# Kernel tuning notes

Measured on AMD Instinct MI355X. Metric: run time of the kernel, lower is better.

The kernel has to match this reference:

```python
import jax, jax.numpy as jnp
import numpy as np

B, T, C = 8, 2048, 1024      # batch, timesteps, input_dim
G, E = 2, 320                # groups_dim, entries_dim
EMB = 512                    # emb_dim
D = EMB // G                 # true_emb_dim per group


def setup_inputs() -> dict:
    key = jax.random.key(0)
    k1, k2, k3 = jax.random.split(key, 3)
    X = jax.random.normal(k1, (B, T, C), dtype=jnp.float32)
    # nn.Linear(input_dim, G*E): weight (out,in) ~ N(0,1), bias zeros
    W = jax.random.normal(k2, (G * E, C), dtype=jnp.float32)
    b = jnp.zeros((G * E,), dtype=jnp.float32)
    # codebook Parameter(1, G*E, D) ~ U[0,1); stored squeezed as (G*E, D)
    codebook = jax.random.uniform(k3, (G * E, D), dtype=jnp.float32)
    return {"X": X, "W": W, "b": b, "codebook": codebook}


def reference(X, W, b, codebook):
    # Eval-mode forward of VectorQuantization (time_first=True).
    nB, nT, _ = X.shape
    logits = jnp.einsum("btc,kc->btk", X, W) + b           # (B, T, G*E)
    # Faithful to source: view (B,T,G*E) as (B*G, T*E) and argmax over last dim
    flat = logits.reshape(nB * G, nT * E)                   # (B*G, T*E)
    k = jnp.argmax(flat, axis=-1)                           # (B*G,)
    hard = jax.nn.one_hot(k, nT * E, dtype=logits.dtype)    # (B*G, T*E)
    q = hard.reshape(nB * nT, G, E)                         # (B*T, G, E)
    # (one-hot * codebook).sum over entries == per-group gather
    cb = codebook.reshape(G, E, D)                          # (G, E, D)
    out = jnp.einsum("nge,ged->ngd", q, cb)                 # (B*T, G, D)
    return out.reshape(nB, nT, G * D)                       # (B, T, emb_dim)
```

## Files before the change

### kernel.cpp

```cpp
#include <hip/hip_runtime.h>
#include <stdint.h>

#define CC    1024
#define EE    320
#define KN    640
#define DD    256
#define MTOT  16384
#define NBLK  640
#define OUT4  2097152
#define MARGIN 2.0f

typedef __attribute__((ext_vector_type(8))) short short8;
typedef __attribute__((ext_vector_type(4))) float f32x4;

__device__ __forceinline__ unsigned int f32_orderable(float x) {
    unsigned int b = __float_as_uint(x);
    return (b & 0x80000000u) ? ~b : (b | 0x80000000u);
}

__device__ __forceinline__ unsigned short bf16_rne(float x) {
    unsigned int u = __float_as_uint(x);
    return (unsigned short)((u + 0x7FFFu + ((u >> 16) & 1u)) >> 16);
}

__global__ void init_slots_kernel(unsigned long long* __restrict__ slots) {
    if (threadIdx.x < 17) slots[threadIdx.x] = 0ull;
}

__global__ __launch_bounds__(256)
void convert_kernel(const float* __restrict__ X, const float* __restrict__ W,
                    unsigned short* __restrict__ A2F, unsigned short* __restrict__ B2F,
                    unsigned long long* __restrict__ slots, float* __restrict__ out) {
    const int bid = blockIdx.x;
    const int tid = threadIdx.x;
    {
        int zidx = bid * 256 + tid;
        f32x4 z = {0.f, 0.f, 0.f, 0.f};
        if (zidx < OUT4) __builtin_nontemporal_store(z, (f32x4*)out + zidx);
    }
    const int lane = tid & 63;
    const float* src;
    unsigned short* dst;
    int unit;
    if (bid < 8192) {
        unit = bid * 4 + (tid >> 6);
        src = X; dst = A2F;
    } else {
        if (bid == 8192 && tid < 17) slots[tid] = 0ull;
        unit = (bid - 8192) * 4 + (tid >> 6);
        src = W; dst = B2F;
    }
    int rt = unit >> 5, kc = unit & 31;
    int row = rt * 16 + (lane & 15);
    int col = kc * 32 + ((lane >> 4) << 3);
    const float* p = src + (size_t)row * CC + col;
    float4 v0 = *(const float4*)p;
    float4 v1 = *(const float4*)(p + 4);
    short8 hi;
    hi[0] = (short)bf16_rne(v0.x); hi[1] = (short)bf16_rne(v0.y);
    hi[2] = (short)bf16_rne(v0.z); hi[3] = (short)bf16_rne(v0.w);
    hi[4] = (short)bf16_rne(v1.x); hi[5] = (short)bf16_rne(v1.y);
    hi[6] = (short)bf16_rne(v1.z); hi[7] = (short)bf16_rne(v1.w);
    *(short8*)(dst + (size_t)unit * 512 + lane * 8) = hi;
}

__global__ __launch_bounds__(256, 3)
void gemm_argmax_mfma(const unsigned short* __restrict__ A2F,
                      const unsigned short* __restrict__ B2F,
                      const float* __restrict__ X,
                      const float* __restrict__ W,
                      const float* __restrict__ bias,
                      const float* __restrict__ codebook,
                      float* __restrict__ out,
                      unsigned long long* __restrict__ slots,
                      unsigned int* __restrict__ counter) {
    __shared__ float redf[4];
    __shared__ int cnt_s;
    __shared__ int cand_s[128];
    __shared__ unsigned int done_s;
    __shared__ unsigned long long s16[16];

    const int tid  = threadIdx.x;
    const int lane = tid & 63;
    const int wave = tid >> 6;

    const int l   = blockIdx.x;
    const int xcd = l & 7;
    const int w   = l >> 3;
    const int mt  = xcd * 16 + w / 5;
    const int nt  = w % 5;
    const int m0 = mt * 128;
    const int n0 = nt * 128;

    const int wm = (wave >> 1) * 64;
    const int wn = (wave & 1) * 64;

    const unsigned short* Ap[4];
    const unsigned short* Bp[4];
#pragma unroll
    for (int t = 0; t < 4; t++) {
        Ap[t] = A2F + ((size_t)(((m0 + wm) >> 4) + t) * 32) * 512 + lane * 8;
        Bp[t] = B2F + ((size_t)(((n0 + wn) >> 4) + t) * 32) * 512 + lane * 8;
    }

    f32x4 acc[4][4] = {};
    short8 a0[4], b0[4], a1[4], b1[4];

#pragma unroll
    for (int t = 0; t < 4; t++) {
        a0[t] = *(const short8*)(Ap[t]);
        b0[t] = *(const short8*)(Bp[t]);
        Ap[t] += 512; Bp[t] += 512;
    }

#define STEP(CURA, CURB, NXTA, NXTB, IT)                                         \
    {                                                                            \
        if ((IT) < 31) {                                                         \
            _Pragma("unroll")                                                    \
            for (int t = 0; t < 4; t++) {                                        \
                NXTA[t] = *(const short8*)(Ap[t]);                               \
                NXTB[t] = *(const short8*)(Bp[t]);                               \
                Ap[t] += 512; Bp[t] += 512;                                      \
            }                                                                    \
        }                                                                        \
        _Pragma("unroll")                                                        \
        for (int ti = 0; ti < 4; ti++)                                           \
            _Pragma("unroll")                                                    \
            for (int tj = 0; tj < 4; tj++)                                       \
                acc[ti][tj] = __builtin_amdgcn_mfma_f32_16x16x32_bf16(           \
                    CURA[ti], CURB[tj], acc[ti][tj], 0, 0, 0);                   \
    }

    for (int it2 = 0; it2 < 16; it2++) {
        STEP(a0, b0, a1, b1, it2 * 2)
        STEP(a1, b1, a0, b0, it2 * 2 + 1)
    }
#undef STEP

    float bias4[4];
#pragma unroll
    for (int tj = 0; tj < 4; tj++) bias4[tj] = bias[n0 + wn + tj * 16 + (lane & 15)];

    float vmax = -3.0e38f;
#pragma unroll
    for (int ti = 0; ti < 4; ti++)
#pragma unroll
        for (int tj = 0; tj < 4; tj++)
#pragma unroll
            for (int r = 0; r < 4; r++)
                vmax = fmaxf(vmax, acc[ti][tj][r] + bias4[tj]);
#pragma unroll
    for (int off = 32; off > 0; off >>= 1)
        vmax = fmaxf(vmax, __shfl_down(vmax, off, 64));
    if (lane == 0) redf[wave] = vmax;
    if (tid == 0) cnt_s = 0;
    __syncthreads();
    float bm = fmaxf(fmaxf(redf[0], redf[1]), fmaxf(redf[2], redf[3]));
    float thresh = bm - MARGIN;

#pragma unroll
    for (int ti = 0; ti < 4; ti++) {
#pragma unroll
        for (int r = 0; r < 4; r++) {
            int m = m0 + wm + ti * 16 + (lane >> 4) * 4 + r;
#pragma unroll
            for (int tj = 0; tj < 4; tj++) {
                float v = acc[ti][tj][r] + bias4[tj];
                if (v >= thresh) {
                    int n = n0 + wn + tj * 16 + (lane & 15);
                    int idx = atomicAdd(&cnt_s, 1);
                    if (idx < 128) cand_s[idx] = (m << 10) | n;
                }
            }
        }
    }
    __syncthreads();
    int cnt = cnt_s < 128 ? cnt_s : 128;

    for (int i = 0; i < cnt; i++) {
        int mc = cand_s[i] >> 10;
        int nc = cand_s[i] & 1023;
        float4 xv = *(const float4*)(X + (size_t)mc * CC + tid * 4);
        float4 wv = *(const float4*)(W + (size_t)nc * CC + tid * 4);
        float p = xv.x * wv.x + xv.y * wv.y + xv.z * wv.z + xv.w * wv.w;
#pragma unroll
        for (int off = 32; off > 0; off >>= 1) p += __shfl_down(p, off, 64);
        if (lane == 0) redf[wave] = p;
        __syncthreads();
        if (tid == 0) {
            float tot = redf[0] + redf[1] + redf[2] + redf[3] + bias[nc];
            unsigned int c = (unsigned int)((mc & 1023) * KN + nc);
            unsigned long long pk =
                ((unsigned long long)f32_orderable(tot) << 32) |
                (unsigned long long)(~c);
            atomicMax(slots + (mc >> 10), pk);
        }
        __syncthreads();
    }

    if (tid == 0) {
        __threadfence();
        done_s = atomicAdd(counter, 1u);
    }
    __syncthreads();

    if (done_s == NBLK - 1) {
        if (tid < 16) s16[tid] = atomicAdd(slots + tid, 0ull);
        __syncthreads();
        int rr  = tid >> 4;
        int seg = tid & 15;
        unsigned long long p = s16[rr];
        unsigned int c = ~(unsigned int)(p & 0xFFFFFFFFull);
        int tl = (int)(c / KN);
        int kg = (int)(c % KN);
        int b  = rr >> 1, h = rr & 1;
        int nstar = b * 2048 + h * 1024 + tl;
        int g = kg / EE;
        const float4* src = (const float4*)(codebook + (size_t)kg * DD) + seg * 4;
        float4* dst = (float4*)(out + (size_t)nstar * 512 + (size_t)g * DD) + seg * 4;
#pragma unroll
        for (int j = 0; j < 4; j++) dst[j] = src[j];
    }
}

__global__ __launch_bounds__(256)
void zs_kernel(const unsigned long long* __restrict__ slots,
               const float* __restrict__ codebook,
               float4* __restrict__ out4) {
    int i4 = blockIdx.x * 256 + threadIdx.x;
    int n  = i4 >> 7;
    int c4 = i4 & 127;
    int b  = n >> 11;
    int h  = (n >> 10) & 1;
    unsigned long long p = slots[b * 2 + h];
    unsigned int c = ~(unsigned int)(p & 0xFFFFFFFFull);
    int tl = (int)(c / KN);
    int kg = (int)(c % KN);
    int nstar = b * 2048 + h * 1024 + tl;
    int g = kg / EE;
    float4 v = make_float4(0.f, 0.f, 0.f, 0.f);
    if (n == nstar && (c4 >> 6) == g)
        v = ((const float4*)codebook)[kg * 64 + (c4 & 63)];
    out4[i4] = v;
}

#define BM 128
#define BN 64
#define BK 32
#define LDA (BM + 4)
#define LDB (BN + 4)

__global__ __launch_bounds__(128)
void gemm_argmax_f32(const float* __restrict__ X, const float* __restrict__ W,
                     const float* __restrict__ bias,
                     unsigned long long* __restrict__ slots) {
    __shared__ float Asf[BK][LDA];
    __shared__ float Bsf[BK][LDB];
    const int tid = threadIdx.x;
    const int m0 = blockIdx.y * BM;
    const int n0 = blockIdx.x * BN;
    const int tx = tid & 7, ty = tid >> 3;
    float acc[8][8];
#pragma unroll
    for (int i = 0; i < 8; i++)
#pragma unroll
        for (int j = 0; j < 8; j++) acc[i][j] = 0.0f;
    const int lm = tid >> 3, lk = (tid & 7) * 4;
    const float* Xb = X + (size_t)m0 * CC;
    const float* Wb = W + (size_t)n0 * CC;
    for (int k0 = 0; k0 < CC; k0 += BK) {
#pragma unroll
        for (int r = 0; r < 8; r++) {
            int m = r * 16 + lm;
            float4 v = *(const float4*)(Xb + (size_t)m * CC + k0 + lk);
            Asf[lk + 0][m] = v.x; Asf[lk + 1][m] = v.y; Asf[lk + 2][m] = v.z; Asf[lk + 3][m] = v.w;
        }
#pragma unroll
        for (int r = 0; r < 4; r++) {
            int m = r * 16 + lm;
            float4 v = *(const float4*)(Wb + (size_t)m * CC + k0 + lk);
            Bsf[lk + 0][m] = v.x; Bsf[lk + 1][m] = v.y; Bsf[lk + 2][m] = v.z; Bsf[lk + 3][m] = v.w;
        }
        __syncthreads();
#pragma unroll
        for (int kk = 0; kk < BK; kk++) {
            float4 A0 = *(const float4*)&Asf[kk][ty * 8];
            float4 A1 = *(const float4*)&Asf[kk][ty * 8 + 4];
            float4 B0 = *(const float4*)&Bsf[kk][tx * 8];
            float4 B1 = *(const float4*)&Bsf[kk][tx * 8 + 4];
            float a[8] = {A0.x, A0.y, A0.z, A0.w, A1.x, A1.y, A1.z, A1.w};
            float b[8] = {B0.x, B0.y, B0.z, B0.w, B1.x, B1.y, B1.z, B1.w};
#pragma unroll
            for (int i = 0; i < 8; i++)
#pragma unroll
                for (int j = 0; j < 8; j++) acc[i][j] = fmaf(a[i], b[j], acc[i][j]);
        }
        __syncthreads();
    }
    unsigned long long best = 0ull;
#pragma unroll
    for (int i = 0; i < 8; i++) {
        int mg = m0 + ty * 8 + i;
        int tl = mg & 1023;
#pragma unroll
        for (int j = 0; j < 8; j++) {
            int kg = n0 + tx * 8 + j;
            float v = acc[i][j] + bias[kg];
            unsigned int c = (unsigned int)(tl * KN + kg);
            unsigned long long p = ((unsigned long long)f32_orderable(v) << 32) |
                                   (unsigned long long)(~c);
            if (p > best) best = p;
        }
    }
#pragma unroll
    for (int off = 32; off > 0; off >>= 1) {
        unsigned long long o = __shfl_down(best, off, 64);
        if (o > best) best = o;
    }
    __shared__ unsigned long long red2[2];
    if ((tid & 63) == 0) red2[tid >> 6] = best;
    __syncthreads();
    if (tid == 0) {
        unsigned long long b0 = red2[0], b1 = red2[1];
        atomicMax(slots + (m0 >> 10), b0 > b1 ? b0 : b1);
    }
}

extern "C" void kernel_launch(void* const* d_in, const int* in_sizes, int n_in,
                              void* d_out, int out_size, void* d_ws, size_t ws_size,
                              hipStream_t stream) {
    const float* X        = (const float*)d_in[0];
    const float* W        = (const float*)d_in[1];
    const float* bias     = (const float*)d_in[2];
    const float* codebook = (const float*)d_in[3];
    float* out = (float*)d_out;

    unsigned long long* slots = (unsigned long long*)d_ws;
    unsigned int* counter = (unsigned int*)(slots + 16);
    const size_t A_off   = 256;
    const size_t A_bytes = (size_t)MTOT * CC * 2;
    const size_t B_off   = A_off + A_bytes;
    const size_t B_bytes = (size_t)KN * CC * 2;
    const size_t need = B_off + B_bytes;

    if (ws_size >= need) {
        unsigned short* A2F = (unsigned short*)((char*)d_ws + A_off);
        unsigned short* B2F = (unsigned short*)((char*)d_ws + B_off);
        hipLaunchKernelGGL(convert_kernel, dim3(8192 + 320), dim3(256), 0, stream,
                           X, W, A2F, B2F, slots, out);
        hipLaunchKernelGGL(gemm_argmax_mfma, dim3(NBLK), dim3(256), 0, stream,
                           A2F, B2F, X, W, bias, codebook, out, slots, counter);
    } else {
        hipLaunchKernelGGL(init_slots_kernel, dim3(1), dim3(64), 0, stream, slots);
        hipLaunchKernelGGL(gemm_argmax_f32, dim3(KN / BN, MTOT / BM), dim3(128), 0, stream,
                           X, W, bias, slots);
        hipLaunchKernelGGL(zs_kernel, dim3(OUT4 / 256), dim3(256), 0, stream,
                           slots, codebook, (float4*)out);
    }
}
```

Before: 154.3 us.

## Fuse X bf16 conversion into GEMM and shrink tiles to 128x64

```diff
diff --git a/kernel.cpp b/kernel.cpp
--- a/kernel.cpp
+++ b/kernel.cpp
@@ -6,7 +6,7 @@
 #define KN    640
 #define DD    256
 #define MTOT  16384
-#define NBLK  640
+#define NBLK  1280
 #define OUT4  2097152
 #define MARGIN 2.0f
 
@@ -23,51 +23,47 @@
     return (unsigned short)((u + 0x7FFFu + ((u >> 16) & 1u)) >> 16);
 }
 
+__device__ __forceinline__ short8 cvt_hi8(float4 a, float4 b) {
+    short8 h;
+    h[0] = (short)bf16_rne(a.x); h[1] = (short)bf16_rne(a.y);
+    h[2] = (short)bf16_rne(a.z); h[3] = (short)bf16_rne(a.w);
+    h[4] = (short)bf16_rne(b.x); h[5] = (short)bf16_rne(b.y);
+    h[6] = (short)bf16_rne(b.z); h[7] = (short)bf16_rne(b.w);
+    return h;
+}
+
 __global__ void init_slots_kernel(unsigned long long* __restrict__ slots) {
     if (threadIdx.x < 17) slots[threadIdx.x] = 0ull;
 }
 
 __global__ __launch_bounds__(256)
-void convert_kernel(const float* __restrict__ X, const float* __restrict__ W,
-                    unsigned short* __restrict__ A2F, unsigned short* __restrict__ B2F,
-                    unsigned long long* __restrict__ slots, float* __restrict__ out) {
+void prep_kernel(const float* __restrict__ W, unsigned short* __restrict__ B2F,
+                 unsigned long long* __restrict__ slots, float* __restrict__ out) {
     const int bid = blockIdx.x;
     const int tid = threadIdx.x;
-    {
-        int zidx = bid * 256 + tid;
-        f32x4 z = {0.f, 0.f, 0.f, 0.f};
-        if (zidx < OUT4) __builtin_nontemporal_store(z, (f32x4*)out + zidx);
-    }
-    const int lane = tid & 63;
-    const float* src;
-    unsigned short* dst;
-    int unit;
-    if (bid < 8192) {
-        unit = bid * 4 + (tid >> 6);
-        src = X; dst = A2F;
-    } else {
-        if (bid == 8192 && tid < 17) slots[tid] = 0ull;
-        unit = (bid - 8192) * 4 + (tid >> 6);
-        src = W; dst = B2F;
-    }
-    int rt = unit >> 5, kc = unit & 31;
-    int row = rt * 16 + (lane & 15);
-    int col = kc * 32 + ((lane >> 4) << 3);
-    const float* p = src + (size_t)row * CC + col;
-    float4 v0 = *(const float4*)p;
-    float4 v1 = *(const float4*)(p + 4);
-    short8 hi;
-    hi[0] = (short)bf16_rne(v0.x); hi[1] = (short)bf16_rne(v0.y);
-    hi[2] = (short)bf16_rne(v0.z); hi[3] = (short)bf16_rne(v0.w);
-    hi[4] = (short)bf16_rne(v1.x); hi[5] = (short)bf16_rne(v1.y);
-    hi[6] = (short)bf16_rne(v1.z); hi[7] = (short)bf16_rne(v1.w);
-    *(short8*)(dst + (size_t)unit * 512 + lane * 8) = hi;
-}
-
-__global__ __launch_bounds__(256, 3)
-void gemm_argmax_mfma(const unsigned short* __restrict__ A2F,
+    f32x4 z = {0.f, 0.f, 0.f, 0.f};
+#pragma unroll
+    for (int ps = 0; ps < 4; ps++) {
+        int zidx = ps * (2048 * 256) + bid * 256 + tid;
+        __builtin_nontemporal_store(z, (f32x4*)out + zidx);
+    }
+    if (bid == 0 && tid < 17) slots[tid] = 0ull;
+    if (bid < 320) {
+        int unit = bid * 4 + (tid >> 6);
+        int lane = tid & 63;
+        int rt = unit >> 5, kc = unit & 31;
+        int row = rt * 16 + (lane & 15);
+        int col = kc * 32 + ((lane >> 4) << 3);
+        const float* p = W + (size_t)row * CC + col;
+        float4 v0 = *(const float4*)p;
+        float4 v1 = *(const float4*)(p + 4);
+        *(short8*)(B2F + (size_t)unit * 512 + lane * 8) = cvt_hi8(v0, v1);
+    }
+}
+
+__global__ __launch_bounds__(256, 4)
+void gemm_argmax_mfma(const float* __restrict__ X,
                       const unsigned short* __restrict__ B2F,
-                      const float* __restrict__ X,
                       const float* __restrict__ W,
                       const float* __restrict__ bias,
                       const float* __restrict__ codebook,
@@ -87,63 +83,79 @@
     const int l   = blockIdx.x;
     const int xcd = l & 7;
     const int w   = l >> 3;
-    const int mt  = xcd * 16 + w / 5;
-    const int nt  = w % 5;
+    const int mt  = xcd * 16 + w / 10;
+    const int nt  = w % 10;
     const int m0 = mt * 128;
-    const int n0 = nt * 128;
-
-    const int wm = (wave >> 1) * 64;
-    const int wn = (wave & 1) * 64;
-
-    const unsigned short* Ap[4];
-    const unsigned short* Bp[4];
-#pragma unroll
-    for (int t = 0; t < 4; t++) {
-        Ap[t] = A2F + ((size_t)(((m0 + wm) >> 4) + t) * 32) * 512 + lane * 8;
-        Bp[t] = B2F + ((size_t)(((n0 + wn) >> 4) + t) * 32) * 512 + lane * 8;
-    }
-
-    f32x4 acc[4][4] = {};
-    short8 a0[4], b0[4], a1[4], b1[4];
-
-#pragma unroll
-    for (int t = 0; t < 4; t++) {
-        a0[t] = *(const short8*)(Ap[t]);
-        b0[t] = *(const short8*)(Bp[t]);
-        Ap[t] += 512; Bp[t] += 512;
+    const int n0 = nt * 64;
+
+    const int rb = m0 + wave * 32;
+    const int fr = lane & 15;
+    const int q  = lane >> 4;
+
+    const float* Axp[2];
+#pragma unroll
+    for (int ti = 0; ti < 2; ti++)
+        Axp[ti] = X + (size_t)(rb + ti * 16 + fr) * CC + q * 8;
+    const unsigned short* Bxp[4];
+#pragma unroll
+    for (int tj = 0; tj < 4; tj++)
+        Bxp[tj] = B2F + ((size_t)((n0 >> 4) + tj) * 32) * 512 + lane * 8;
+
+    f32x4 acc[2][4] = {};
+    float4 af0[2][2], af1[2][2];
+    short8 bb0[4], bb1[4];
+
+#pragma unroll
+    for (int ti = 0; ti < 2; ti++) {
+        af0[ti][0] = *(const float4*)(Axp[ti]);
+        af0[ti][1] = *(const float4*)(Axp[ti] + 4);
+        Axp[ti] += 32;
+    }
+#pragma unroll
+    for (int tj = 0; tj < 4; tj++) {
+        bb0[tj] = *(const short8*)(Bxp[tj]);
+        Bxp[tj] += 512;
     }
 
 #define STEP(CURA, CURB, NXTA, NXTB, IT)                                         \
     {                                                                            \
         if ((IT) < 31) {                                                         \
             _Pragma("unroll")                                                    \
-            for (int t = 0; t < 4; t++) {                                        \
-                NXTA[t] = *(const short8*)(Ap[t]);                               \
-                NXTB[t] = *(const short8*)(Bp[t]);                               \
-                Ap[t] += 512; Bp[t] += 512;                                      \
+            for (int ti = 0; ti < 2; ti++) {                                     \
+                NXTA[ti][0] = *(const float4*)(Axp[ti]);                         \
+                NXTA[ti][1] = *(const float4*)(Axp[ti] + 4);                     \
+                Axp[ti] += 32;                                                   \
+            }                                                                    \
+            _Pragma("unroll")                                                    \
+            for (int tj = 0; tj < 4; tj++) {                                     \
+                NXTB[tj] = *(const short8*)(Bxp[tj]);                            \
+                Bxp[tj] += 512;                                                  \
             }                                                                    \
         }                                                                        \
+        short8 ah[2];                                                            \
         _Pragma("unroll")                                                        \
-        for (int ti = 0; ti < 4; ti++)                                           \
+        for (int ti = 0; ti < 2; ti++) ah[ti] = cvt_hi8(CURA[ti][0], CURA[ti][1]); \
+        _Pragma("unroll")                                                        \
+        for (int ti = 0; ti < 2; ti++)                                           \
             _Pragma("unroll")                                                    \
             for (int tj = 0; tj < 4; tj++)                                       \
                 acc[ti][tj] = __builtin_amdgcn_mfma_f32_16x16x32_bf16(           \
-                    CURA[ti], CURB[tj], acc[ti][tj], 0, 0, 0);                   \
+                    ah[ti], CURB[tj], acc[ti][tj], 0, 0, 0);                     \
     }
 
     for (int it2 = 0; it2 < 16; it2++) {
-        STEP(a0, b0, a1, b1, it2 * 2)
-        STEP(a1, b1, a0, b0, it2 * 2 + 1)
+        STEP(af0, bb0, af1, bb1, it2 * 2)
+        STEP(af1, bb1, af0, bb0, it2 * 2 + 1)
     }
 #undef STEP
 
     float bias4[4];
 #pragma unroll
-    for (int tj = 0; tj < 4; tj++) bias4[tj] = bias[n0 + wn + tj * 16 + (lane & 15)];
+    for (int tj = 0; tj < 4; tj++) bias4[tj] = bias[n0 + tj * 16 + (lane & 15)];
 
     float vmax = -3.0e38f;
 #pragma unroll
-    for (int ti = 0; ti < 4; ti++)
+    for (int ti = 0; ti < 2; ti++)
 #pragma unroll
         for (int tj = 0; tj < 4; tj++)
 #pragma unroll
@@ -159,15 +171,15 @@
     float thresh = bm - MARGIN;
 
 #pragma unroll
-    for (int ti = 0; ti < 4; ti++) {
+    for (int ti = 0; ti < 2; ti++) {
 #pragma unroll
         for (int r = 0; r < 4; r++) {
-            int m = m0 + wm + ti * 16 + (lane >> 4) * 4 + r;
+            int m = rb + ti * 16 + (lane >> 4) * 4 + r;
 #pragma unroll
             for (int tj = 0; tj < 4; tj++) {
                 float v = acc[ti][tj][r] + bias4[tj];
                 if (v >= thresh) {
-                    int n = n0 + wn + tj * 16 + (lane & 15);
+                    int n = n0 + tj * 16 + (lane & 15);
                     int idx = atomicAdd(&cnt_s, 1);
                     if (idx < 128) cand_s[idx] = (m << 10) | n;
                 }
@@ -337,19 +349,16 @@
 
     unsigned long long* slots = (unsigned long long*)d_ws;
     unsigned int* counter = (unsigned int*)(slots + 16);
-    const size_t A_off   = 256;
-    const size_t A_bytes = (size_t)MTOT * CC * 2;
-    const size_t B_off   = A_off + A_bytes;
+    const size_t B_off   = 256;
     const size_t B_bytes = (size_t)KN * CC * 2;
     const size_t need = B_off + B_bytes;
 
     if (ws_size >= need) {
-        unsigned short* A2F = (unsigned short*)((char*)d_ws + A_off);
         unsigned short* B2F = (unsigned short*)((char*)d_ws + B_off);
-        hipLaunchKernelGGL(convert_kernel, dim3(8192 + 320), dim3(256), 0, stream,
-                           X, W, A2F, B2F, slots, out);
+        hipLaunchKernelGGL(prep_kernel, dim3(2048), dim3(256), 0, stream,
+                           W, B2F, slots, out);
         hipLaunchKernelGGL(gemm_argmax_mfma, dim3(NBLK), dim3(256), 0, stream,
-                           A2F, B2F, X, W, bias, codebook, out, slots, counter);
+                           X, B2F, W, bias, codebook, out, slots, counter);
     } else {
         hipLaunchKernelGGL(init_slots_kernel, dim3(1), dim3(64), 0, stream, slots);
         hipLaunchKernelGGL(gemm_argmax_f32, dim3(KN / BN, MTOT / BM), dim3(128), 0, stream,
```

New measurement: 242.4 us. +57.1%, slower.

## Halve GEMM tile width to 128x64 and double block count for occupancy

Applied to the files above, without the earlier changes.

```diff
diff --git a/kernel.cpp b/kernel.cpp
--- a/kernel.cpp
+++ b/kernel.cpp
@@ -6,7 +6,7 @@
 #define KN    640
 #define DD    256
 #define MTOT  16384
-#define NBLK  640
+#define NBLK  1280
 #define OUT4  2097152
 #define MARGIN 2.0f
 
@@ -64,7 +64,7 @@
     *(short8*)(dst + (size_t)unit * 512 + lane * 8) = hi;
 }
 
-__global__ __launch_bounds__(256, 3)
+__global__ __launch_bounds__(256, 4)
 void gemm_argmax_mfma(const unsigned short* __restrict__ A2F,
                       const unsigned short* __restrict__ B2F,
                       const float* __restrict__ X,
@@ -87,44 +87,44 @@
     const int l   = blockIdx.x;
     const int xcd = l & 7;
     const int w   = l >> 3;
-    const int mt  = xcd * 16 + w / 5;
-    const int nt  = w % 5;
+    const int mt  = xcd * 16 + w / 10;
+    const int nt  = w % 10;
     const int m0 = mt * 128;
-    const int n0 = nt * 128;
-
-    const int wm = (wave >> 1) * 64;
-    const int wn = (wave & 1) * 64;
-
-    const unsigned short* Ap[4];
+    const int n0 = nt * 64;
+
+    const int rb = m0 + wave * 32;
+
+    const unsigned short* Ap[2];
     const unsigned short* Bp[4];
 #pragma unroll
-    for (int t = 0; t < 4; t++) {
-        Ap[t] = A2F + ((size_t)(((m0 + wm) >> 4) + t) * 32) * 512 + lane * 8;
-        Bp[t] = B2F + ((size_t)(((n0 + wn) >> 4) + t) * 32) * 512 + lane * 8;
-    }
-
-    f32x4 acc[4][4] = {};
-    short8 a0[4], b0[4], a1[4], b1[4];
-
-#pragma unroll
-    for (int t = 0; t < 4; t++) {
-        a0[t] = *(const short8*)(Ap[t]);
-        b0[t] = *(const short8*)(Bp[t]);
-        Ap[t] += 512; Bp[t] += 512;
-    }
+    for (int ti = 0; ti < 2; ti++)
+        Ap[ti] = A2F + ((size_t)((rb >> 4) + ti) * 32) * 512 + lane * 8;
+#pragma unroll
+    for (int tj = 0; tj < 4; tj++)
+        Bp[tj] = B2F + ((size_t)((n0 >> 4) + tj) * 32) * 512 + lane * 8;
+
+    f32x4 acc[2][4] = {};
+    short8 a0[2], b0[4], a1[2], b1[4];
+
+#pragma unroll
+    for (int ti = 0; ti < 2; ti++) { a0[ti] = *(const short8*)(Ap[ti]); Ap[ti] += 512; }
+#pragma unroll
+    for (int tj = 0; tj < 4; tj++) { b0[tj] = *(const short8*)(Bp[tj]); Bp[tj] += 512; }
 
 #define STEP(CURA, CURB, NXTA, NXTB, IT)                                         \
     {                                                                            \
         if ((IT) < 31) {                                                         \
             _Pragma("unroll")                                                    \
-            for (int t = 0; t < 4; t++) {                                        \
-                NXTA[t] = *(const short8*)(Ap[t]);                               \
-                NXTB[t] = *(const short8*)(Bp[t]);                               \
-                Ap[t] += 512; Bp[t] += 512;                                      \
+            for (int ti = 0; ti < 2; ti++) {                                     \
+                NXTA[ti] = *(const short8*)(Ap[ti]); Ap[ti] += 512;              \
+            }                                                                    \
+            _Pragma("unroll")                                                    \
+            for (int tj = 0; tj < 4; tj++) {                                     \
+                NXTB[tj] = *(const short8*)(Bp[tj]); Bp[tj] += 512;              \
             }                                                                    \
         }                                                                        \
         _Pragma("unroll")                                                        \
-        for (int ti = 0; ti < 4; ti++)                                           \
+        for (int ti = 0; ti < 2; ti++)                                           \
             _Pragma("unroll")                                                    \
             for (int tj = 0; tj < 4; tj++)                                       \
                 acc[ti][tj] = __builtin_amdgcn_mfma_f32_16x16x32_bf16(           \
@@ -139,11 +139,11 @@
 
     float bias4[4];
 #pragma unroll
-    for (int tj = 0; tj < 4; tj++) bias4[tj] = bias[n0 + wn + tj * 16 + (lane & 15)];
+    for (int tj = 0; tj < 4; tj++) bias4[tj] = bias[n0 + tj * 16 + (lane & 15)];
 
     float vmax = -3.0e38f;
 #pragma unroll
-    for (int ti = 0; ti < 4; ti++)
+    for (int ti = 0; ti < 2; ti++)
 #pragma unroll
         for (int tj = 0; tj < 4; tj++)
 #pragma unroll
@@ -159,15 +159,15 @@
     float thresh = bm - MARGIN;
 
 #pragma unroll
-    for (int ti = 0; ti < 4; ti++) {
+    for (int ti = 0; ti < 2; ti++) {
 #pragma unroll
         for (int r = 0; r < 4; r++) {
-            int m = m0 + wm + ti * 16 + (lane >> 4) * 4 + r;
+            int m = rb + ti * 16 + (lane >> 4) * 4 + r;
 #pragma unroll
             for (int tj = 0; tj < 4; tj++) {
                 float v = acc[ti][tj][r] + bias4[tj];
                 if (v >= thresh) {
-                    int n = n0 + wn + tj * 16 + (lane & 15);
+                    int n = n0 + tj * 16 + (lane & 15);
                     int idx = atomicAdd(&cnt_s, 1);
                     if (idx < 128) cand_s[idx] = (m << 10) | n;
                 }
```

Measured after the change: 186.0 us. 1.21x slower.
